# Kernel optimization log

Measured on AMD Instinct MI355X. Metric: run time of the kernel, lower is better.

The kernel has to match this reference:

```python
import jax, jax.numpy as jnp
import numpy as np

# ---- Clifford algebra Cl(3,0): 8 blades ordered by grade: [1, e1,e2,e3, e12,e13,e23, e123] ----
_ORDER = [0, 1, 2, 4, 3, 5, 6, 7]  # bitmask of each blade in grade-sorted order
GRADES = np.array([0, 1, 1, 1, 2, 2, 2, 3])  # grade (subspace) of each blade
EPS = 1e-6

def _build_cayley():
    C = np.zeros((8, 8, 8), np.float32)
    for ia, a in enumerate(_ORDER):
        for ib, b in enumerate(_ORDER):
            # reordering sign from anticommuting basis vectors (Euclidean metric -> squares +1)
            t, tot = a >> 1, 0
            while t:
                tot += bin(t & b).count("1")
                t >>= 1
            s = 1.0 if tot % 2 == 0 else -1.0
            C[ia, ib, _ORDER.index(a ^ b)] = s
    return jnp.asarray(C)

CAYLEY = _build_cayley()  # [8,8,8], highly sparse (64 nonzeros)

def mvlinear(x, W, b):
    # x: [B,N,Cin,8], W: [Cout,Cin,4] per-grade weights, b: [Cout] bias on scalar blade
    Wf = W[:, :, GRADES]                               # [Cout,Cin,8] via repeat over grades [1,3,3,1]
    y = jnp.einsum("bnci,oci->bnoi", x, Wf)
    return y.at[..., 0].add(b)

def setup_inputs() -> dict:
    key = jax.random.key(0)
    ks = jax.random.split(key, 5)
    B, N, Cin, Ch = 8, 4096, 64, 128
    return {
        "x": jax.random.normal(ks[0], (B, N, Cin, 8), jnp.float32),
        "W1": jax.random.normal(ks[1], (Ch, Cin, 4), jnp.float32) / np.sqrt(Cin),
        "b1": jax.random.normal(ks[2], (Ch,), jnp.float32) * 0.02,
        "W2": jax.random.normal(ks[3], (Cin, Ch, 4), jnp.float32) / np.sqrt(Ch),
        "b2": jax.random.normal(ks[4], (Cin,), jnp.float32) * 0.02,
        "a": jnp.ones((Cin,), jnp.float32),
    }

def reference(x, W1, b1, W2, b2, a):
    h = mvlinear(x, W1, b1)                                   # [B,N,Ch,8]
    h = jnp.einsum("bnci,ijk,bncj->bnck", h, CAYLEY, h)       # geometric product (sparse Cayley)
    y = mvlinear(h, W2, b2)                                   # [B,N,Cin,8]
    # MVLayerNorm: per-channel multivector norm (Euclidean: sqrt(sum of squares)),
    # averaged over channels, then scale by learned a
    norm = jnp.sqrt(jnp.sum(y * y, axis=-1, keepdims=True))   # [B,N,Cin,1]
    denom = jnp.mean(norm, axis=-2, keepdims=True) + EPS      # [B,N,1,1]
    return a[None, None, :, None] * y / denom
```

## Files before the change

### kernel.cpp

```cpp
#include <hip/hip_runtime.h>
#include <stdint.h>

typedef unsigned short u16;
typedef __attribute__((ext_vector_type(4))) float f32x4;
typedef __attribute__((ext_vector_type(8))) __bf16 bf16x8;

struct Cay { int idx[8][8]; float sgn[8][8]; };
constexpr int kOrder[8] = {0,1,2,4,3,5,6,7};
constexpr int ordpos(int m){ int r=-1; for(int i=0;i<8;i++) if(kOrder[i]==m) r=i; return r; }
constexpr Cay make_cay(){
  Cay c{};
  for(int ia=0; ia<8; ia++) for(int ib=0; ib<8; ib++){
    int a=kOrder[ia], b=kOrder[ib];
    int t=a>>1, tot=0;
    while(t){ int x=t&b; while(x){ tot+=x&1; x>>=1; } t>>=1; }
    c.idx[ia][ib]=ordpos(a^b);
    c.sgn[ia][ib]=(tot&1)?-1.0f:1.0f;
  }
  return c;
}
constexpr Cay CAY = make_cay();

struct GPTab { float dsgn[8]; int np; int pi[28]; int pj[28]; int pk[28]; float ps[28]; };
constexpr GPTab make_gptab(){
  GPTab t{};
  for (int i=0;i<8;i++) t.dsgn[i] = CAY.sgn[i][i];
  t.np = 0;
  for (int i=0;i<8;i++) for (int j=i+1;j<8;j++){
    float s = CAY.sgn[i][j] + CAY.sgn[j][i];
    if (s != 0.0f){ t.pi[t.np]=i; t.pj[t.np]=j; t.pk[t.np]=CAY.idx[i][j]; t.ps[t.np]=s; t.np++; }
  }
  return t;
}
constexpr GPTab GPT = make_gptab();

__device__ __forceinline__ void gprod(const float* h, float* g){
  float g0 = h[0]*h[0];
  #pragma unroll
  for (int i=1;i<8;i++) g0 = fmaf(GPT.dsgn[i]>0.f ? h[i] : -h[i], h[i], g0);
  g[0] = g0;
  #pragma unroll
  for (int k=1;k<8;k++) g[k] = 0.f;
  #pragma unroll
  for (int t=0;t<GPT.np;t++)
    g[GPT.pk[t]] = fmaf(GPT.ps[t]*h[GPT.pi[t]], h[GPT.pj[t]], g[GPT.pk[t]]);
}

__device__ __forceinline__ u16 f2bf(float f){
  union { float f; uint32_t u; } v; v.f=f;
  uint32_t u=v.u;
  return (u16)((u + 0x7fffu + ((u>>16)&1u)) >> 16);
}

__device__ __forceinline__ uint32_t cvtpk(float lo, float hi){
  uint32_t r;
  asm("v_cvt_pk_bf16_f32 %0, %1, %2" : "=v"(r) : "v"(lo), "v"(hi));
  return r;
}

__global__ void gp_prepack(const float* __restrict__ W1, const float* __restrict__ W2,
                           u16* __restrict__ w1p, u16* __restrict__ w2p)
{
  int t = blockIdx.x*256 + threadIdx.x;
  int e = t & 7, l = (t>>3)&63, f = t>>9;
  int lm = l & 15, lh = l >> 4;
  if (f < 64) {
    int g = f >> 4, ks = (f>>3)&1, ot = f&7;
    int o = ot*16 + lm, c = ks*32 + lh*8 + e;
    w1p[f*512 + l*8 + e] = f2bf(W1[(o*64 + c)*4 + g]);
  } else {
    int f2 = f - 64;
    int g = f2 >> 4, ks = (f2>>2)&3, ot = f2&3;
    int outc = ot*16 + lm, o = ks*32 + lh*8 + e;
    w2p[f2*512 + l*8 + e] = f2bf(W2[(outc*128 + o)*4 + g]);
  }
}

__global__ __launch_bounds__(256,4) void gp_fused(
    const float* __restrict__ x, const u16* __restrict__ w1p,
    const float* __restrict__ b1, const u16* __restrict__ w2p,
    const float* __restrict__ b2, const float* __restrict__ avec,
    float* __restrict__ out)
{
  __shared__ __align__(16) char SH[32768];
  __shared__ float redArr[16][4];
  __shared__ float denomArr[16];

  const int tid = threadIdx.x;
  const int w  = tid >> 6;
  const int l  = tid & 63;
  const int lm = l & 15;
  const int lh = l >> 4;
  const int xk = (lm & 7) << 4;

  {
    const int cp = tid & 31;
    const int pr = tid >> 5;
    const float4* xt = reinterpret_cast<const float4*>(x) + (size_t)blockIdx.x * 2048;
    #pragma unroll
    for (int it=0; it<2; ++it){
      const int p = pr + it*8;
      const float4* src = xt + p*128 + cp*4;
      float4 v0 = src[0], v1 = src[1], v2 = src[2], v3 = src[3];
      uint32_t pk[8];
      pk[0]=cvtpk(v0.x,v2.x); pk[1]=cvtpk(v0.y,v2.y); pk[2]=cvtpk(v0.z,v2.z); pk[3]=cvtpk(v0.w,v2.w);
      pk[4]=cvtpk(v1.x,v3.x); pk[5]=cvtpk(v1.y,v3.y); pk[6]=cvtpk(v1.z,v3.z); pk[7]=cvtpk(v1.w,v3.w);
      const int xo = (p & 7) << 4;
      #pragma unroll
      for (int b=0;b<8;b++)
        *reinterpret_cast<uint32_t*>(SH + ((((p*8+b)<<7) + (cp<<2)) ^ xo)) = pk[b];
    }
  }
  __syncthreads();

  constexpr int BSTART[4] = {0,1,4,7};
  constexpr int BCNT[4]   = {1,3,3,1};

  f32x4 acc1[2][8];
  #pragma unroll
  for (int cc=0; cc<2; ++cc)
    #pragma unroll
    for (int b=0; b<8; ++b)
      acc1[cc][b] = (f32x4){0.f,0.f,0.f,0.f};

  const uint4* w1f = reinterpret_cast<const uint4*>(w1p);
  #pragma unroll
  for (int g4=0; g4<4; ++g4){
    #pragma unroll
    for (int ks=0; ks<2; ++ks){
      uint4 wa = w1f[((g4*2+ks)*8 + w    )*64 + l];
      uint4 wb = w1f[((g4*2+ks)*8 + w + 4)*64 + l];
      bf16x8 wav = __builtin_bit_cast(bf16x8, wa);
      bf16x8 wbv = __builtin_bit_cast(bf16x8, wb);
      #pragma unroll
      for (int bi=0; bi<3; ++bi){
        if (bi >= BCNT[g4]) break;
        const int blade = BSTART[g4] + bi;
        bf16x8 xv = *reinterpret_cast<const bf16x8*>(
            SH + ((((lm*8+blade)<<7) + ((ks*32+lh*8)<<1)) ^ xk));
        acc1[0][blade] = __builtin_amdgcn_mfma_f32_16x16x32_bf16(wav, xv, acc1[0][blade], 0,0,0);
        acc1[1][blade] = __builtin_amdgcn_mfma_f32_16x16x32_bf16(wbv, xv, acc1[1][blade], 0,0,0);
      }
    }
  }
  __syncthreads();

  #pragma unroll
  for (int cc=0; cc<2; ++cc){
    const int cht = w + cc*4;
    const float4 b14 = reinterpret_cast<const float4*>(b1)[cht*4 + lh];
    const float bb[4] = {b14.x, b14.y, b14.z, b14.w};
    uint32_t lo[8], hi[8];
    #pragma unroll
    for (int rp=0; rp<2; ++rp){
      float ga[8], gb[8];
      {
        float h[8];
        #pragma unroll
        for (int b=0;b<8;b++) h[b] = acc1[cc][b][rp*2+0];
        h[0] += bb[rp*2+0];
        gprod(h, ga);
      }
      {
        float h[8];
        #pragma unroll
        for (int b=0;b<8;b++) h[b] = acc1[cc][b][rp*2+1];
        h[0] += bb[rp*2+1];
        gprod(h, gb);
      }
      #pragma unroll
      for (int b=0;b<8;b++){
        uint32_t v = cvtpk(ga[b], gb[b]);
        if (rp==0) lo[b] = v; else hi[b] = v;
      }
    }
    const int chByte = (cht*16 + lh*4) << 1;
    #pragma unroll
    for (int b=0;b<8;b++){
      uint2 v; v.x = lo[b]; v.y = hi[b];
      *reinterpret_cast<uint2*>(SH + ((((lm*8+b)<<8) + chByte) ^ xk)) = v;
    }
  }
  __syncthreads();

  f32x4 acc2[8];
  #pragma unroll
  for (int b=0; b<8; ++b) acc2[b] = (f32x4){0.f,0.f,0.f,0.f};

  const uint4* w2f = reinterpret_cast<const uint4*>(w2p);
  #pragma unroll
  for (int ks=0; ks<4; ++ks){
    #pragma unroll
    for (int g4=0; g4<4; ++g4){
      uint4 wu = w2f[((g4*4+ks)*4 + w)*64 + l];
      bf16x8 wv = __builtin_bit_cast(bf16x8, wu);
      #pragma unroll
      for (int bi=0; bi<3; ++bi){
        if (bi >= BCNT[g4]) break;
        const int blade = BSTART[g4] + bi;
        bf16x8 gv = *reinterpret_cast<const bf16x8*>(
            SH + ((((lm*8+blade)<<8) + ((ks*32+lh*8)<<1)) ^ xk));
        acc2[blade] = __builtin_amdgcn_mfma_f32_16x16x32_bf16(gv, wv, acc2[blade], 0,0,0);
      }
    }
  }

  const int oc = w*16 + lm;
  const float b2v  = b2[oc];
  const float aval = avec[oc];
  #pragma unroll
  for (int r=0; r<4; ++r) acc2[0][r] += b2v;

  float nrm[4];
  #pragma unroll
  for (int r=0; r<4; ++r) {
    float s = 0.f;
    #pragma unroll
    for (int b=0; b<8; ++b) s = fmaf(acc2[b][r], acc2[b][r], s);
    nrm[r] = sqrtf(s);
  }
  #pragma unroll
  for (int r=0; r<4; ++r) {
    float v = nrm[r];
    v += __shfl_xor(v, 1, 64);
    v += __shfl_xor(v, 2, 64);
    v += __shfl_xor(v, 4, 64);
    v += __shfl_xor(v, 8, 64);
    nrm[r] = v;
  }
  if (lm == 0) {
    #pragma unroll
    for (int r=0; r<4; ++r) redArr[lh*4 + r][w] = nrm[r];
  }
  __syncthreads();
  if (tid < 16)
    denomArr[tid] = (redArr[tid][0]+redArr[tid][1]+redArr[tid][2]+redArr[tid][3])
                    * (1.0f/64.0f) + 1e-6f;
  __syncthreads();

  #pragma unroll
  for (int r=0; r<4; ++r) {
    const int pos = lh*4 + r;
    const float sc = aval / denomArr[pos];
    float4 o0, o1;
    o0.x = acc2[0][r]*sc; o0.y = acc2[1][r]*sc; o0.z = acc2[2][r]*sc; o0.w = acc2[3][r]*sc;
    o1.x = acc2[4][r]*sc; o1.y = acc2[5][r]*sc; o1.z = acc2[6][r]*sc; o1.w = acc2[7][r]*sc;
    size_t P = (size_t)blockIdx.x*16 + pos;
    float4* op = reinterpret_cast<float4*>(out + (P*64 + (size_t)oc)*8);
    op[0] = o0; op[1] = o1;
  }
}

extern "C" void kernel_launch(void* const* d_in, const int* in_sizes, int n_in,
                              void* d_out, int out_size, void* d_ws, size_t ws_size,
                              hipStream_t stream)
{
  const float* x  = (const float*)d_in[0];
  const float* W1 = (const float*)d_in[1];
  const float* b1 = (const float*)d_in[2];
  const float* W2 = (const float*)d_in[3];
  const float* b2 = (const float*)d_in[4];
  const float* a  = (const float*)d_in[5];
  float* out = (float*)d_out;

  u16* w1p = (u16*)d_ws;
  u16* w2p = w1p + 32768;

  gp_prepack<<<256, 256, 0, stream>>>(W1, W2, w1p, w2p);
  gp_fused<<<2048, 256, 0, stream>>>(x, w1p, b1, w2p, b2, a, out);
}
```

Before: 43.84 us.

## Process two tiles per block with register prefetch of next x tile

Each block now handles two 16-position tiles in a loop, prefetching the second tile's x data into registers while the first tile computes. Separate shared regions for x and intermediate products remove one barrier per tile. The factor of 2 on symmetric geometric-product terms is folded into the prepacked W2 weights, and the denominator reduction is done per thread instead of through an extra shared array and barrier. Launch bounds drop to 3 waves per SIMD, and the grid is halved, which raises register and LDS use per block and reduces parallelism.

```diff
diff --git a/kernel.cpp b/kernel.cpp
--- a/kernel.cpp
+++ b/kernel.cpp
@@ -28,13 +28,14 @@
   t.np = 0;
   for (int i=0;i<8;i++) for (int j=i+1;j<8;j++){
     float s = CAY.sgn[i][j] + CAY.sgn[j][i];
-    if (s != 0.0f){ t.pi[t.np]=i; t.pj[t.np]=j; t.pk[t.np]=CAY.idx[i][j]; t.ps[t.np]=s; t.np++; }
+    if (s != 0.0f){ t.pi[t.np]=i; t.pj[t.np]=j; t.pk[t.np]=CAY.idx[i][j];
+                    t.ps[t.np]=(s>0.f)?1.0f:-1.0f; t.np++; }
   }
   return t;
 }
 constexpr GPTab GPT = make_gptab();
 
-__device__ __forceinline__ void gprod(const float* h, float* g){
+__device__ __forceinline__ void gprod_half(const float* h, float* g){
   float g0 = h[0]*h[0];
   #pragma unroll
   for (int i=1;i<8;i++) g0 = fmaf(GPT.dsgn[i]>0.f ? h[i] : -h[i], h[i], g0);
@@ -43,7 +44,8 @@
   for (int k=1;k<8;k++) g[k] = 0.f;
   #pragma unroll
   for (int t=0;t<GPT.np;t++)
-    g[GPT.pk[t]] = fmaf(GPT.ps[t]*h[GPT.pi[t]], h[GPT.pj[t]], g[GPT.pk[t]]);
+    g[GPT.pk[t]] = fmaf(GPT.ps[t]>0.f ? h[GPT.pi[t]] : -h[GPT.pi[t]],
+                        h[GPT.pj[t]], g[GPT.pk[t]]);
 }
 
 __device__ __forceinline__ u16 f2bf(float f){
@@ -72,19 +74,22 @@
     int f2 = f - 64;
     int g = f2 >> 4, ks = (f2>>2)&3, ot = f2&3;
     int outc = ot*16 + lm, o = ks*32 + lh*8 + e;
-    w2p[f2*512 + l*8 + e] = f2bf(W2[(outc*128 + o)*4 + g]);
-  }
-}
-
-__global__ __launch_bounds__(256,4) void gp_fused(
+    float sc = (g == 0) ? 1.0f : 2.0f;
+    w2p[f2*512 + l*8 + e] = f2bf(W2[(outc*128 + o)*4 + g] * sc);
+  }
+}
+
+#define X_OFF 0
+#define G_OFF 16384
+
+__global__ __launch_bounds__(256,3) void gp_fused(
     const float* __restrict__ x, const u16* __restrict__ w1p,
     const float* __restrict__ b1, const u16* __restrict__ w2p,
     const float* __restrict__ b2, const float* __restrict__ avec,
     float* __restrict__ out)
 {
-  __shared__ __align__(16) char SH[32768];
+  __shared__ __align__(16) char SH[49152];
   __shared__ float redArr[16][4];
-  __shared__ float denomArr[16];
 
   const int tid = threadIdx.x;
   const int w  = tid >> 6;
@@ -92,162 +97,182 @@
   const int lm = l & 15;
   const int lh = l >> 4;
   const int xk = (lm & 7) << 4;
-
+  const int cp = tid & 31;
+  const int pr = tid >> 5;
+
+  constexpr int BSTART[4] = {0,1,4,7};
+  constexpr int BCNT[4]   = {1,3,3,1};
+
+  const float4* xb = reinterpret_cast<const float4*>(x);
+  const uint4* w1f = reinterpret_cast<const uint4*>(w1p);
+  const uint4* w2f = reinterpret_cast<const uint4*>(w2p);
+
+  float4 rx[8];
   {
-    const int cp = tid & 31;
-    const int pr = tid >> 5;
-    const float4* xt = reinterpret_cast<const float4*>(x) + (size_t)blockIdx.x * 2048;
+    const float4* s0 = xb + (size_t)blockIdx.x * 4096;
+    #pragma unroll
+    for (int it=0; it<2; ++it){
+      const float4* s = s0 + (pr + it*8)*128 + cp*4;
+      rx[it*4+0]=s[0]; rx[it*4+1]=s[1]; rx[it*4+2]=s[2]; rx[it*4+3]=s[3];
+    }
+  }
+
+  #pragma unroll 1
+  for (int t=0; t<2; ++t){
+    const size_t tile = (size_t)blockIdx.x*2 + t;
+
     #pragma unroll
     for (int it=0; it<2; ++it){
       const int p = pr + it*8;
-      const float4* src = xt + p*128 + cp*4;
-      float4 v0 = src[0], v1 = src[1], v2 = src[2], v3 = src[3];
+      float4 v0=rx[it*4+0], v1=rx[it*4+1], v2=rx[it*4+2], v3=rx[it*4+3];
+      if (it==1) { v0=rx[4]; v1=rx[5]; v2=rx[6]; v3=rx[7]; }
       uint32_t pk[8];
       pk[0]=cvtpk(v0.x,v2.x); pk[1]=cvtpk(v0.y,v2.y); pk[2]=cvtpk(v0.z,v2.z); pk[3]=cvtpk(v0.w,v2.w);
       pk[4]=cvtpk(v1.x,v3.x); pk[5]=cvtpk(v1.y,v3.y); pk[6]=cvtpk(v1.z,v3.z); pk[7]=cvtpk(v1.w,v3.w);
       const int xo = (p & 7) << 4;
       #pragma unroll
       for (int b=0;b<8;b++)
-        *reinterpret_cast<uint32_t*>(SH + ((((p*8+b)<<7) + (cp<<2)) ^ xo)) = pk[b];
-    }
-  }
-  __syncthreads();
-
-  constexpr int BSTART[4] = {0,1,4,7};
-  constexpr int BCNT[4]   = {1,3,3,1};
-
-  f32x4 acc1[2][8];
-  #pragma unroll
-  for (int cc=0; cc<2; ++cc)
-    #pragma unroll
-    for (int b=0; b<8; ++b)
-      acc1[cc][b] = (f32x4){0.f,0.f,0.f,0.f};
-
-  const uint4* w1f = reinterpret_cast<const uint4*>(w1p);
-  #pragma unroll
-  for (int g4=0; g4<4; ++g4){
-    #pragma unroll
-    for (int ks=0; ks<2; ++ks){
-      uint4 wa = w1f[((g4*2+ks)*8 + w    )*64 + l];
-      uint4 wb = w1f[((g4*2+ks)*8 + w + 4)*64 + l];
-      bf16x8 wav = __builtin_bit_cast(bf16x8, wa);
-      bf16x8 wbv = __builtin_bit_cast(bf16x8, wb);
-      #pragma unroll
-      for (int bi=0; bi<3; ++bi){
-        if (bi >= BCNT[g4]) break;
-        const int blade = BSTART[g4] + bi;
-        bf16x8 xv = *reinterpret_cast<const bf16x8*>(
-            SH + ((((lm*8+blade)<<7) + ((ks*32+lh*8)<<1)) ^ xk));
-        acc1[0][blade] = __builtin_amdgcn_mfma_f32_16x16x32_bf16(wav, xv, acc1[0][blade], 0,0,0);
-        acc1[1][blade] = __builtin_amdgcn_mfma_f32_16x16x32_bf16(wbv, xv, acc1[1][blade], 0,0,0);
-      }
-    }
-  }
-  __syncthreads();
-
-  #pragma unroll
-  for (int cc=0; cc<2; ++cc){
-    const int cht = w + cc*4;
-    const float4 b14 = reinterpret_cast<const float4*>(b1)[cht*4 + lh];
-    const float bb[4] = {b14.x, b14.y, b14.z, b14.w};
-    uint32_t lo[8], hi[8];
-    #pragma unroll
-    for (int rp=0; rp<2; ++rp){
-      float ga[8], gb[8];
-      {
-        float h[8];
+        *reinterpret_cast<uint32_t*>(SH + X_OFF + ((((p*8+b)<<7) + (cp<<2)) ^ xo)) = pk[b];
+    }
+    __syncthreads();
+
+    if (t == 0){
+      const float4* s1 = xb + ((size_t)blockIdx.x*2 + 1) * 2048;
+      #pragma unroll
+      for (int it=0; it<2; ++it){
+        const float4* s = s1 + (pr + it*8)*128 + cp*4;
+        rx[it*4+0]=s[0]; rx[it*4+1]=s[1]; rx[it*4+2]=s[2]; rx[it*4+3]=s[3];
+      }
+    }
+
+    f32x4 acc1[2][8];
+    #pragma unroll
+    for (int cc=0; cc<2; ++cc)
+      #pragma unroll
+      for (int b=0; b<8; ++b)
+        acc1[cc][b] = (f32x4){0.f,0.f,0.f,0.f};
+
+    #pragma unroll
+    for (int g4=0; g4<4; ++g4){
+      #pragma unroll
+      for (int ks=0; ks<2; ++ks){
+        uint4 wa = w1f[((g4*2+ks)*8 + w    )*64 + l];
+        uint4 wb = w1f[((g4*2+ks)*8 + w + 4)*64 + l];
+        bf16x8 wav = __builtin_bit_cast(bf16x8, wa);
+        bf16x8 wbv = __builtin_bit_cast(bf16x8, wb);
         #pragma unroll
-        for (int b=0;b<8;b++) h[b] = acc1[cc][b][rp*2+0];
-        h[0] += bb[rp*2+0];
-        gprod(h, ga);
-      }
-      {
-        float h[8];
+        for (int bi=0; bi<3; ++bi){
+          if (bi >= BCNT[g4]) break;
+          const int blade = BSTART[g4] + bi;
+          bf16x8 xv = *reinterpret_cast<const bf16x8*>(
+              SH + X_OFF + ((((lm*8+blade)<<7) + ((ks*32+lh*8)<<1)) ^ xk));
+          acc1[0][blade] = __builtin_amdgcn_mfma_f32_16x16x32_bf16(wav, xv, acc1[0][blade], 0,0,0);
+          acc1[1][blade] = __builtin_amdgcn_mfma_f32_16x16x32_bf16(wbv, xv, acc1[1][blade], 0,0,0);
+        }
+      }
+    }
+
+    #pragma unroll
+    for (int cc=0; cc<2; ++cc){
+      const int cht = w + cc*4;
+      const float4 b14 = reinterpret_cast<const float4*>(b1)[cht*4 + lh];
+      const float bb[4] = {b14.x, b14.y, b14.z, b14.w};
+      uint32_t lo[8], hi[8];
+      #pragma unroll
+      for (int rp=0; rp<2; ++rp){
+        float ga[8], gb[8];
+        {
+          float h[8];
+          #pragma unroll
+          for (int b=0;b<8;b++) h[b] = acc1[cc][b][rp*2+0];
+          h[0] += bb[rp*2+0];
+          gprod_half(h, ga);
+        }
+        {
+          float h[8];
+          #pragma unroll
+          for (int b=0;b<8;b++) h[b] = acc1[cc][b][rp*2+1];
+          h[0] += bb[rp*2+1];
+          gprod_half(h, gb);
+        }
         #pragma unroll
-        for (int b=0;b<8;b++) h[b] = acc1[cc][b][rp*2+1];
-        h[0] += bb[rp*2+1];
-        gprod(h, gb);
-      }
+        for (int b=0;b<8;b++){
+          uint32_t v = cvtpk(ga[b], gb[b]);
+          if (rp==0) lo[b] = v; else hi[b] = v;
+        }
+      }
+      const int chByte = (cht*16 + lh*4) << 1;
       #pragma unroll
       for (int b=0;b<8;b++){
-        uint32_t v = cvtpk(ga[b], gb[b]);
-        if (rp==0) lo[b] = v; else hi[b] = v;
-      }
-    }
-    const int chByte = (cht*16 + lh*4) << 1;
-    #pragma unroll
-    for (int b=0;b<8;b++){
-      uint2 v; v.x = lo[b]; v.y = hi[b];
-      *reinterpret_cast<uint2*>(SH + ((((lm*8+b)<<8) + chByte) ^ xk)) = v;
-    }
-  }
-  __syncthreads();
-
-  f32x4 acc2[8];
-  #pragma unroll
-  for (int b=0; b<8; ++b) acc2[b] = (f32x4){0.f,0.f,0.f,0.f};
-
-  const uint4* w2f = reinterpret_cast<const uint4*>(w2p);
-  #pragma unroll
-  for (int ks=0; ks<4; ++ks){
-    #pragma unroll
-    for (int g4=0; g4<4; ++g4){
-      uint4 wu = w2f[((g4*4+ks)*4 + w)*64 + l];
-      bf16x8 wv = __builtin_bit_cast(bf16x8, wu);
-      #pragma unroll
-      for (int bi=0; bi<3; ++bi){
-        if (bi >= BCNT[g4]) break;
-        const int blade = BSTART[g4] + bi;
-        bf16x8 gv = *reinterpret_cast<const bf16x8*>(
-            SH + ((((lm*8+blade)<<8) + ((ks*32+lh*8)<<1)) ^ xk));
-        acc2[blade] = __builtin_amdgcn_mfma_f32_16x16x32_bf16(gv, wv, acc2[blade], 0,0,0);
-      }
-    }
-  }
-
-  const int oc = w*16 + lm;
-  const float b2v  = b2[oc];
-  const float aval = avec[oc];
-  #pragma unroll
-  for (int r=0; r<4; ++r) acc2[0][r] += b2v;
-
-  float nrm[4];
-  #pragma unroll
-  for (int r=0; r<4; ++r) {
-    float s = 0.f;
-    #pragma unroll
-    for (int b=0; b<8; ++b) s = fmaf(acc2[b][r], acc2[b][r], s);
-    nrm[r] = sqrtf(s);
-  }
-  #pragma unroll
-  for (int r=0; r<4; ++r) {
-    float v = nrm[r];
-    v += __shfl_xor(v, 1, 64);
-    v += __shfl_xor(v, 2, 64);
-    v += __shfl_xor(v, 4, 64);
-    v += __shfl_xor(v, 8, 64);
-    nrm[r] = v;
-  }
-  if (lm == 0) {
-    #pragma unroll
-    for (int r=0; r<4; ++r) redArr[lh*4 + r][w] = nrm[r];
-  }
-  __syncthreads();
-  if (tid < 16)
-    denomArr[tid] = (redArr[tid][0]+redArr[tid][1]+redArr[tid][2]+redArr[tid][3])
-                    * (1.0f/64.0f) + 1e-6f;
-  __syncthreads();
-
-  #pragma unroll
-  for (int r=0; r<4; ++r) {
-    const int pos = lh*4 + r;
-    const float sc = aval / denomArr[pos];
-    float4 o0, o1;
-    o0.x = acc2[0][r]*sc; o0.y = acc2[1][r]*sc; o0.z = acc2[2][r]*sc; o0.w = acc2[3][r]*sc;
-    o1.x = acc2[4][r]*sc; o1.y = acc2[5][r]*sc; o1.z = acc2[6][r]*sc; o1.w = acc2[7][r]*sc;
-    size_t P = (size_t)blockIdx.x*16 + pos;
-    float4* op = reinterpret_cast<float4*>(out + (P*64 + (size_t)oc)*8);
-    op[0] = o0; op[1] = o1;
+        uint2 v; v.x = lo[b]; v.y = hi[b];
+        *reinterpret_cast<uint2*>(SH + G_OFF + (((lm*8+b)<<8) + (chByte ^ xk))) = v;
+      }
+    }
+    __syncthreads();
+
+    f32x4 acc2[8];
+    #pragma unroll
+    for (int b=0; b<8; ++b) acc2[b] = (f32x4){0.f,0.f,0.f,0.f};
+
+    #pragma unroll
+    for (int ks=0; ks<4; ++ks){
+      #pragma unroll
+      for (int g4=0; g4<4; ++g4){
+        uint4 wu = w2f[((g4*4+ks)*4 + w)*64 + l];
+        bf16x8 wv = __builtin_bit_cast(bf16x8, wu);
+        #pragma unroll
+        for (int bi=0; bi<3; ++bi){
+          if (bi >= BCNT[g4]) break;
+          const int blade = BSTART[g4] + bi;
+          bf16x8 gv = *reinterpret_cast<const bf16x8*>(
+              SH + G_OFF + (((lm*8+blade)<<8) + (((ks*64+lh*16)) ^ xk)));
+          acc2[blade] = __builtin_amdgcn_mfma_f32_16x16x32_bf16(gv, wv, acc2[blade], 0,0,0);
+        }
+      }
+    }
+
+    const int oc = w*16 + lm;
+    const float b2v  = b2[oc];
+    const float aval = avec[oc];
+    #pragma unroll
+    for (int r=0; r<4; ++r) acc2[0][r] += b2v;
+
+    float nrm[4];
+    #pragma unroll
+    for (int r=0; r<4; ++r) {
+      float s = 0.f;
+      #pragma unroll
+      for (int b=0; b<8; ++b) s = fmaf(acc2[b][r], acc2[b][r], s);
+      nrm[r] = sqrtf(s);
+    }
+    #pragma unroll
+    for (int r=0; r<4; ++r) {
+      float v = nrm[r];
+      v += __shfl_xor(v, 1, 64);
+      v += __shfl_xor(v, 2, 64);
+      v += __shfl_xor(v, 4, 64);
+      v += __shfl_xor(v, 8, 64);
+      nrm[r] = v;
+    }
+    if (lm == 0) {
+      #pragma unroll
+      for (int r=0; r<4; ++r) redArr[lh*4 + r][w] = nrm[r];
+    }
+    __syncthreads();
+
+    #pragma unroll
+    for (int r=0; r<4; ++r) {
+      const int pos = lh*4 + r;
+      const float4 rr = *reinterpret_cast<const float4*>(redArr[pos]);
+      const float denom = (rr.x+rr.y+rr.z+rr.w) * (1.0f/64.0f) + 1e-6f;
+      const float sc = aval / denom;
+      float4 o0, o1;
+      o0.x = acc2[0][r]*sc; o0.y = acc2[1][r]*sc; o0.z = acc2[2][r]*sc; o0.w = acc2[3][r]*sc;
+      o1.x = acc2[4][r]*sc; o1.y = acc2[5][r]*sc; o1.z = acc2[6][r]*sc; o1.w = acc2[7][r]*sc;
+      size_t P = tile*16 + pos;
+      float4* op = reinterpret_cast<float4*>(out + (P*64 + (size_t)oc)*8);
+      op[0] = o0; op[1] = o1;
+    }
   }
 }
 
@@ -267,5 +292,5 @@
   u16* w2p = w1p + 32768;
 
   gp_prepack<<<256, 256, 0, stream>>>(W1, W2, w1p, w2p);
-  gp_fused<<<2048, 256, 0, stream>>>(x, w1p, b1, w2p, b2, a, out);
-}
+  gp_fused<<<1024, 256, 0, stream>>>(x, w1p, b1, w2p, b2, a, out);
+}
```

Measured after the change: 103.9 us. 137% more time.
